# Performance work log

Measured on AMD Instinct MI355X. Metric: run time of the kernel, lower is better.

Reference implementation:

```python
import jax, jax.numpy as jnp
import numpy as np

B, D_INPUT, D_MODEL, MEM, HID, N_SYNCH, OUT_DIMS, ITERS = 128, 512, 2048, 25, 32, 256, 1000, 24
SYNC = N_SYNCH * (N_SYNCH + 1) // 2  # 32896


def setup_inputs() -> dict:
    key = jax.random.key(0)
    ks = jax.random.split(key, 12)
    inp = {
        'x': jax.random.normal(ks[0], (B, D_INPUT), jnp.float32),
        'syn_w': jax.random.normal(ks[1], (D_INPUT + D_MODEL, 2 * D_MODEL), jnp.float32) * 0.02,
        'syn_b': jnp.zeros((2 * D_MODEL,), jnp.float32),
        'ln_g': jnp.ones((D_MODEL,), jnp.float32),
        'ln_b': jnp.zeros((D_MODEL,), jnp.float32),
        'tp_w1': jax.random.normal(ks[2], (MEM, 2 * HID, D_MODEL), jnp.float32) * (1.0 / np.sqrt(MEM + 2 * HID)),
        'tp_b1': jnp.zeros((1, D_MODEL, 2 * HID), jnp.float32),
        'tp_w2': jax.random.normal(ks[3], (HID, 2, D_MODEL), jnp.float32) * (1.0 / np.sqrt(HID + 2)),
        'tp_b2': jnp.zeros((1, D_MODEL, 2), jnp.float32),
        'start_activated_state': jax.random.normal(ks[4], (D_MODEL,), jnp.float32) * (1.0 / np.sqrt(D_MODEL)),
        'start_trace': jax.random.normal(ks[5], (D_MODEL, MEM), jnp.float32) * (1.0 / np.sqrt(D_MODEL + MEM)),
        'decay_params_out': jax.random.uniform(ks[6], (SYNC,), jnp.float32),
        'out_w': jax.random.normal(ks[7], (SYNC, OUT_DIMS), jnp.float32) * 0.02,
        'out_b': jnp.zeros((OUT_DIMS,), jnp.float32),
        'idx_left': jax.random.randint(ks[8], (N_SYNCH,), 0, D_MODEL),
        'idx_right': jax.random.randint(ks[9], (N_SYNCH,), 0, D_MODEL),
        'iterations': ITERS,
    }
    return inp


def _glu(z):
    a, b = jnp.split(z, 2, axis=-1)
    return a * jax.nn.sigmoid(b)


def reference(x, syn_w, syn_b, ln_g, ln_b, tp_w1, tp_b1, tp_w2, tp_b2,
              start_activated_state, start_trace, decay_params_out, out_w, out_b,
              idx_left, idx_right, iterations):
    Bx = x.shape[0]
    D, M = start_trace.shape
    n_synch = idx_left.shape[0]
    iu, ju = np.triu_indices(n_synch)
    r = jnp.exp(-jnp.clip(decay_params_out, 0.0, 15.0))[None, :]  # (1, S)
    log_nc = np.log(out_b.shape[0]).astype(np.float32)

    def pairwise(act):  # act: (B, D) -> (B, S) upper-tri of outer product of selected neurons
        l = act[:, idx_left]
        rr = act[:, idx_right]
        outer = l[:, :, None] * rr[:, None, :]
        return outer[:, iu, ju]

    def trace_proc(trace):  # (B, D, M) -> (B, D) per-neuron MLP (NLM)
        h = _glu(jnp.einsum('BDM,MHD->BDH', trace, tp_w1) + tp_b1)
        o = _glu(jnp.einsum('BDH,HOD->BDO', h, tp_w2) + tp_b2)
        return o[..., 0]

    def layernorm(z):
        mu = jnp.mean(z, -1, keepdims=True)
        var = jnp.mean((z - mu) ** 2, -1, keepdims=True)
        return (z - mu) * jax.lax.rsqrt(var + 1e-5) * ln_g + ln_b

    act0 = jnp.broadcast_to(start_activated_state[None, :], (Bx, D))
    trace0 = jnp.broadcast_to(start_trace[None, :, :], (Bx, D, M))
    alpha0 = pairwise(act0)
    beta0 = jnp.ones_like(alpha0)

    def step(carry, _):
        trace, act, alpha, beta = carry
        pre = jnp.concatenate([x, act], axis=-1)
        state = layernorm(_glu(pre @ syn_w + syn_b))            # (B, D)
        trace = jnp.concatenate([trace[:, :, 1:], state[:, :, None]], axis=-1)
        act = trace_proc(trace)                                  # (B, D)
        pp = pairwise(act)
        alpha = r * alpha + pp
        beta = r * beta + 1.0
        sync = alpha / jnp.sqrt(beta)                            # (B, S)
        pred = sync @ out_w + out_b                              # (B, out)
        logp = jax.nn.log_softmax(pred, axis=-1)
        ne = -jnp.sum(jnp.exp(logp) * logp, axis=-1) / log_nc
        cert = jnp.stack([ne, 1.0 - ne], axis=-1)                # (B, 2)
        return (trace, act, alpha, beta), (pred, cert)

    _, (preds, certs) = jax.lax.scan(step, (trace0, act0, alpha0, beta0), None, length=iterations)
    predictions = jnp.moveaxis(preds, 0, -1)   # (B, out_dims, T)
    certainties = jnp.moveaxis(certs, 0, -1)   # (B, 2, T)
    return predictions, certainties
```

## Files before the change

### kernel.cpp

```cpp
#include <hip/hip_runtime.h>
#include <stdint.h>

#define BB      128
#define DIN     512
#define DMODEL  2048
#define MEMN    25
#define NSY     256
#define OUTD    1000
#define ITERS   24
#define SYNCN   32896
#define KPAD    33792
#define NPAD    1024
#define NSPLIT  32
#define KCH     1056
#define PREDTOT (BB*OUTD*ITERS)

typedef __attribute__((ext_vector_type(8))) short bf16x8;
typedef __attribute__((ext_vector_type(4))) float f32x4;

__device__ __forceinline__ unsigned short f2bf(float x){
    unsigned int u = __float_as_uint(x);
    u += 0x7fffu + ((u >> 16) & 1u);
    return (unsigned short)(u >> 16);
}
__device__ __forceinline__ float bf2f(unsigned short h){
    unsigned int u = ((unsigned int)h) << 16;
    return __uint_as_float(u);
}
__device__ __forceinline__ float sigm(float x){ return 1.f/(1.f + __expf(-x)); }

__device__ __forceinline__ void gload16(const unsigned short* g, unsigned short* l){
    __builtin_amdgcn_global_load_lds(
        (const __attribute__((address_space(1))) unsigned int*)(const void*)g,
        (__attribute__((address_space(3))) unsigned int*)(void*)l,
        16, 0, 0);
}

__device__ __forceinline__ void reduce_row(const float* __restrict__ part, const float* __restrict__ outb,
    float* __restrict__ dout, float* red, int b, int t, int tid){
    float v[4];
    float m = -1e30f;
#pragma unroll
    for (int q = 0; q < 4; ++q){
        int n = q*256 + tid;
        float s;
        if (n < OUTD){
            s = outb[n];
            for (int sk = 0; sk < NSPLIT; ++sk)
                s += part[(long)sk*(BB*NPAD) + (long)b*NPAD + n];
        } else s = -1e30f;
        v[q] = s;
        m = fmaxf(m, s);
    }
#pragma unroll
    for (int off = 32; off; off >>= 1) m = fmaxf(m, __shfl_down(m, off));
    int w = tid >> 6;
    if ((tid & 63) == 0) red[w] = m;
    __syncthreads();
    float M = fmaxf(fmaxf(red[0], red[1]), fmaxf(red[2], red[3]));
    __syncthreads();
    float z = 0.f, s2 = 0.f;
#pragma unroll
    for (int q = 0; q < 4; ++q){
        int n = q*256 + tid;
        if (n < OUTD){
            float e = __expf(v[q] - M);
            z += e; s2 += e*v[q];
        }
    }
#pragma unroll
    for (int off = 32; off; off >>= 1){
        z  += __shfl_down(z, off);
        s2 += __shfl_down(s2, off);
    }
    if ((tid & 63) == 0){ red[w] = z; red[4+w] = s2; }
    __syncthreads();
    if (tid == 0){
        float Z = red[0]+red[1]+red[2]+red[3];
        float S = red[4]+red[5]+red[6]+red[7];
        float logZ = M + __logf(Z);
        float ne = (logZ - S/Z) / 6.907755278982137f;
        dout[PREDTOT + b*48 + t] = ne;
        dout[PREDTOT + b*48 + 24 + t] = 1.f - ne;
    }
#pragma unroll
    for (int q = 0; q < 4; ++q){
        int n = q*256 + tid;
        if (n < OUTD) dout[(long)b*(OUTD*ITERS) + (long)n*ITERS + t] = v[q];
    }
}


__global__ __launch_bounds__(256) void init_trace_k(const float* __restrict__ st,
    unsigned short* __restrict__ trh, unsigned short* __restrict__ trl){
    const long N = (long)MEMN*DMODEL*BB;
    for (long i = (long)blockIdx.x*256 + threadIdx.x; i < N; i += (long)gridDim.x*256){
        int m = (int)(i / (DMODEL*BB));
        int rem = (int)(i % (DMODEL*BB));
        int d = rem >> 7;
        float v = st[d*MEMN + m];
        unsigned short h = f2bf(v);
        trh[i] = h;
        trl[i] = f2bf(v - bf2f(h));
    }
}

__global__ __launch_bounds__(256) void init_act_k(const float* __restrict__ sas, float* __restrict__ act){
    for (int i = blockIdx.x*256 + threadIdx.x; i < DMODEL*BB; i += gridDim.x*256)
        act[i] = sas[i >> 7];
}

__global__ __launch_bounds__(256) void init_alpha_k(const float* __restrict__ sas,
    const int* __restrict__ il, const int* __restrict__ ir, float* __restrict__ alpha){
    int i = blockIdx.x, tid = threadIdx.x;
    if (tid >= NSY - i) return;
    int j = i + tid;
    int k = i*(2*NSY - i + 1)/2 + tid;
    float a0 = sas[il[i]] * sas[ir[j]];
    for (int b = 0; b < BB; ++b) alpha[b*SYNCN + k] = a0;
}

__global__ __launch_bounds__(256) void init_rowmap_k(int* __restrict__ rowOf, int* __restrict__ rowstart){
    int i = blockIdx.x, tid = threadIdx.x;
    int start = i*(2*NSY - i + 1)/2;
    int len = NSY - i;
    if (tid == 0) rowstart[i] = start;
    for (int t = tid; t < len; t += 256) rowOf[start + t] = i;
}

__global__ __launch_bounds__(256) void transpose_f32_k(const float* __restrict__ in, float* __restrict__ out, int R, int C){
    __shared__ float S[64][65];
    int r0 = blockIdx.y*64, c0 = blockIdx.x*64;
    for (int i = threadIdx.x; i < 64*64; i += 256){
        int rr = i >> 6, cc = i & 63;
        int r = r0+rr, c = c0+cc;
        if (r < R && c < C) S[rr][cc] = in[(long)r*C + c];
    }
    __syncthreads();
    for (int i = threadIdx.x; i < 64*64; i += 256){
        int cc = i >> 6, rr = i & 63;
        int r = r0+rr, c = c0+cc;
        if (r < R && c < C) out[(long)c*R + r] = S[rr][cc];
    }
}

__global__ __launch_bounds__(256) void w1bf_prep_k(const float* __restrict__ w1t, unsigned short* __restrict__ w1bf){
    int d = blockIdx.x, tid = threadIdx.x;
    __shared__ float S[1600];
    for (int i = tid; i < 1600; i += 256) S[i] = w1t[(long)d*1600 + i];
    __syncthreads();
    for (int i = tid; i < 2048; i += 256){
        int h = i >> 5, m = i & 31;
        float v = (m < MEMN) ? S[m*64 + h] : 0.f;
        unsigned short hi = f2bf(v);
        unsigned short lo = f2bf(v - bf2f(hi));
        w1bf[(long)d*4096 + i]        = hi;
        w1bf[(long)d*4096 + 2048 + i] = lo;
    }
}

__global__ __launch_bounds__(256) void wbf_transpose_k(const float* __restrict__ w, unsigned short* __restrict__ wt){
    __shared__ float S[64][65];
    int k0 = blockIdx.x*64, n0 = blockIdx.y*64;
    int tid = threadIdx.x;
    if (k0 >= SYNCN){
        uint4 z = {0u,0u,0u,0u};
#pragma unroll
        for (int p = 0; p < 2; ++p){
            int i = tid + p*256;
            int nn = i >> 3, k8 = (i & 7)*8;
            *(uint4*)(wt + (long)(n0+nn)*KPAD + k0 + k8) = z;
        }
        return;
    }
    const long MAXI = (long)SYNCN*OUTD - 4;
#pragma unroll
    for (int p = 0; p < 4; ++p){
        int i = tid + p*256;
        int rr = i >> 4, c4 = (i & 15)*4;
        long idx = (long)(k0+rr)*OUTD + n0 + c4;
        if (idx > MAXI) idx = MAXI;
        float4 v = *(const float4*)(w + idx);
        S[rr][c4+0]=v.x; S[rr][c4+1]=v.y; S[rr][c4+2]=v.z; S[rr][c4+3]=v.w;
    }
    __syncthreads();
#pragma unroll
    for (int p = 0; p < 4; ++p){
        int i = tid + p*256;
        int nn = i >> 4, k4 = (i & 15)*4;
        ushort4 o;
        o.x = f2bf(S[k4+0][nn]); o.y = f2bf(S[k4+1][nn]);
        o.z = f2bf(S[k4+2][nn]); o.w = f2bf(S[k4+3][nn]);
        *(ushort4*)(wt + (long)(n0+nn)*KPAD + k0 + k4) = o;
    }
}

__global__ __launch_bounds__(256) void swt_convert_k(const float* __restrict__ w,
    unsigned short* __restrict__ th, unsigned short* __restrict__ tl){
    __shared__ float S[64][65];
    int k0 = blockIdx.x*64, n0 = blockIdx.y*64;
    int tid = threadIdx.x;
#pragma unroll
    for (int p = 0; p < 4; ++p){
        int i = tid + p*256;
        int rr = i >> 4, c4 = (i & 15)*4;
        float4 v = *(const float4*)(w + (long)(512 + k0 + rr)*4096 + n0 + c4);
        S[rr][c4+0]=v.x; S[rr][c4+1]=v.y; S[rr][c4+2]=v.z; S[rr][c4+3]=v.w;
    }
    __syncthreads();
#pragma unroll
    for (int p = 0; p < 4; ++p){
        int i = tid + p*256;
        int nn = i >> 4, k4 = (i & 15)*4;
        ushort4 oh, ol;
        float v0 = S[k4+0][nn], v1 = S[k4+1][nn], v2 = S[k4+2][nn], v3 = S[k4+3][nn];
        oh.x = f2bf(v0); oh.y = f2bf(v1); oh.z = f2bf(v2); oh.w = f2bf(v3);
        ol.x = f2bf(v0 - bf2f(oh.x)); ol.y = f2bf(v1 - bf2f(oh.y));
        ol.z = f2bf(v2 - bf2f(oh.z)); ol.w = f2bf(v3 - bf2f(oh.w));
        *(ushort4*)(th + (long)(n0+nn)*DMODEL + k0 + k4) = oh;
        *(ushort4*)(tl + (long)(n0+nn)*DMODEL + k0 + k4) = ol;
    }
}

__global__ __launch_bounds__(256) void act_convert_k(const float* __restrict__ act,
    unsigned short* __restrict__ th, unsigned short* __restrict__ tl){
    __shared__ float S[64][65];
    int d0 = blockIdx.x*64, b0 = blockIdx.y*64;
    int tid = threadIdx.x;
#pragma unroll
    for (int p = 0; p < 4; ++p){
        int i = tid + p*256;
        int rr = i >> 4, c4 = (i & 15)*4;
        float4 v = *(const float4*)(act + (long)(d0+rr)*BB + b0 + c4);
        S[rr][c4+0]=v.x; S[rr][c4+1]=v.y; S[rr][c4+2]=v.z; S[rr][c4+3]=v.w;
    }
    __syncthreads();
#pragma unroll
    for (int p = 0; p < 4; ++p){
        int i = tid + p*256;
        int nn = i >> 4, k4 = (i & 15)*4;
        unsigned short h[4], l[4];
#pragma unroll
        for (int q = 0; q < 4; ++q){
            float v = S[k4+q][nn];
            h[q] = f2bf(v);
            l[q] = f2bf(v - bf2f(h[q]));
        }
        *(ushort4*)(th + (long)(b0+nn)*DMODEL + d0 + k4) = ushort4{h[0],h[1],h[2],h[3]};
        *(ushort4*)(tl + (long)(b0+nn)*DMODEL + d0 + k4) = ushort4{l[0],l[1],l[2],l[3]};
    }
}

__global__ __launch_bounds__(256) void gemm_syn_k(const float* __restrict__ A, const float* __restrict__ Bw,
    const float* __restrict__ bias, float* __restrict__ out){
    int j_base = blockIdx.x*64;
    int tid = threadIdx.x;
    __shared__ float As[16][128];
    __shared__ float Bs[16][68];
    int bg = tid & 15, jg = tid >> 4;
    int b0 = bg*8, j0 = jg*4;
    float acc[8][4];
#pragma unroll
    for (int i = 0; i < 8; ++i)
#pragma unroll
        for (int q = 0; q < 4; ++q) acc[i][q] = 0.f;
    for (int kt = 0; kt < 32; ++kt){
        {
            int i0 = tid*8;
            int kk = i0 >> 7, bb = i0 & 127;
            const float4* src = (const float4*)(A + (long)(kt*16+kk)*BB + bb);
            float4 v0 = src[0], v1 = src[1];
            *(float4*)&As[kk][bb]   = v0;
            *(float4*)&As[kk][bb+4] = v1;
        }
        {
            int i0 = tid*4;
            int kk = i0 >> 6, jj = i0 & 63;
            float4 v = *(const float4*)(Bw + (long)(kt*16+kk)*4096 + j_base + jj);
            *(float4*)&Bs[kk][jj] = v;
        }
        __syncthreads();
#pragma unroll
        for (int kk = 0; kk < 16; ++kk){
            float a[8], bv[4];
            *(float4*)&a[0] = *(float4*)&As[kk][b0];
            *(float4*)&a[4] = *(float4*)&As[kk][b0+4];
            *(float4*)&bv[0] = *(float4*)&Bs[kk][j0];
#pragma unroll
            for (int i = 0; i < 8; ++i)
#pragma unroll
                for (int q = 0; q < 4; ++q) acc[i][q] += a[i]*bv[q];
        }
        __syncthreads();
    }
#pragma unroll
    for (int i = 0; i < 8; ++i){
        int bb = b0 + i;
        float4 v;
        v.x = acc[i][0]+bias[j_base+j0+0]; v.y = acc[i][1]+bias[j_base+j0+1];
        v.z = acc[i][2]+bias[j_base+j0+2]; v.w = acc[i][3]+bias[j_base+j0+3];
        *(float4*)(out + (long)bb*4096 + j_base + j0) = v;
    }
}


__global__ __launch_bounds__(256) void mfma_pair_k(
    const unsigned short* __restrict__ Ah, const unsigned short* __restrict__ Al,
    const unsigned short* __restrict__ Bh, const unsigned short* __restrict__ Bl,
    float* __restrict__ zpart,
    const unsigned short* __restrict__ Abf, const unsigned short* __restrict__ Bbf,
    float* __restrict__ part, int has_out){
    __shared__ __align__(16) unsigned short smem[12288];
    int tid = threadIdx.x;
    int bid = blockIdx.x;
    int wid = tid >> 6, lane = tid & 63;
    int wm = (wid & 1)*64, wn = (wid >> 1)*32;
    int mrow = lane & 15, kq = lane >> 4;
    int srow = tid >> 2;
    int ksg  = (tid & 3)*8;

    if (bid < 512){
        unsigned short* As_h = smem;
        unsigned short* As_l = smem + 4096;
        unsigned short* Bs_h = smem + 8192;
        unsigned short* Bs_l = smem + 10240;
        int nb = bid & 63;
        int s  = bid >> 6;

        f32x4 c[4][2];
#pragma unroll
        for (int a = 0; a < 4; ++a)
#pragma unroll
            for (int b = 0; b < 2; ++b) c[a][b] = (f32x4){0.f,0.f,0.f,0.f};

        long koff0 = (long)s*256 + ksg;
        const unsigned short* gAh1 = Ah + (long)srow*DMODEL      + koff0;
        const unsigned short* gAh2 = Ah + (long)(srow+64)*DMODEL + koff0;
        const unsigned short* gAl1 = Al + (long)srow*DMODEL      + koff0;
        const unsigned short* gAl2 = Al + (long)(srow+64)*DMODEL + koff0;
        const unsigned short* gBh  = Bh + (long)(nb*64+srow)*DMODEL + koff0;
        const unsigned short* gBl  = Bl + (long)(nb*64+srow)*DMODEL + koff0;
        unsigned short* lAh1 = As_h + wid*512;
        unsigned short* lAh2 = As_h + 2048 + wid*512;
        unsigned short* lAl1 = As_l + wid*512;
        unsigned short* lAl2 = As_l + 2048 + wid*512;
        unsigned short* lBh  = Bs_h + wid*512;
        unsigned short* lBl  = Bs_l + wid*512;

        for (int ks = 0; ks < 8; ++ks){
            int o = ks*32;
            gload16(gAh1 + o, lAh1);
            gload16(gAh2 + o, lAh2);
            gload16(gAl1 + o, lAl1);
            gload16(gAl2 + o, lAl2);
            gload16(gBh  + o, lBh);
            gload16(gBl  + o, lBl);
            __syncthreads();
            bf16x8 ah[4], al[4], bh[2], bl[2];
#pragma unroll
            for (int x = 0; x < 4; ++x){
                ah[x] = *(const bf16x8*)&As_h[(wm + x*16 + mrow)*32 + kq*8];
                al[x] = *(const bf16x8*)&As_l[(wm + x*16 + mrow)*32 + kq*8];
            }
#pragma unroll
            for (int y = 0; y < 2; ++y){
                bh[y] = *(const bf16x8*)&Bs_h[(wn + y*16 + mrow)*32 + kq*8];
                bl[y] = *(const bf16x8*)&Bs_l[(wn + y*16 + mrow)*32 + kq*8];
            }
#pragma unroll
            for (int a = 0; a < 4; ++a)
#pragma unroll
                for (int b = 0; b < 2; ++b){
                    c[a][b] = __builtin_amdgcn_mfma_f32_16x16x32_bf16(ah[a], bh[b], c[a][b], 0, 0, 0);
                    c[a][b] = __builtin_amdgcn_mfma_f32_16x16x32_bf16(al[a], bh[b], c[a][b], 0, 0, 0);
                    c[a][b] = __builtin_amdgcn_mfma_f32_16x16x32_bf16(ah[a], bl[b], c[a][b], 0, 0, 0);
                }
            __syncthreads();
        }
        float* outp = zpart + (long)s*(BB*4096);
#pragma unroll
        for (int a = 0; a < 4; ++a)
#pragma unroll
            for (int b = 0; b < 2; ++b){
                int r0 = wm + a*16 + (lane >> 4)*4;
                int col = nb*64 + wn + b*16 + (lane & 15);
#pragma unroll
                for (int reg = 0; reg < 4; ++reg)
                    outp[(long)(r0+reg)*4096 + col] = c[a][b][reg];
            }
    } else {
        if (!has_out) return;
        unsigned short* As = smem;
        unsigned short* Bs = smem + 4096;
        int idx = bid - 512;
        int sk = idx >> 4;
        int n_base = (idx & 15)*64;
        long k_base = (long)sk*KCH;

        f32x4 c[4][2];
#pragma unroll
        for (int a = 0; a < 4; ++a)
#pragma unroll
            for (int b = 0; b < 2; ++b) c[a][b] = (f32x4){0.f,0.f,0.f,0.f};

        const unsigned short* gA1 = Abf + (long)srow*KPAD      + k_base + ksg;
        const unsigned short* gA2 = Abf + (long)(srow+64)*KPAD + k_base + ksg;
        const unsigned short* gB  = Bbf + (long)(n_base+srow)*KPAD + k_base + ksg;
        unsigned short* lA1 = As + wid*512;
        unsigned short* lA2 = As + 2048 + wid*512;
        unsigned short* lB  = Bs + wid*512;

        for (int ks = 0; ks < KCH/32; ++ks){
            int o = ks*32;
            gload16(gA1 + o, lA1);
            gload16(gA2 + o, lA2);
            gload16(gB  + o, lB);
            __syncthreads();
            bf16x8 af[4], bf[2];
#pragma unroll
            for (int x = 0; x < 4; ++x)
                af[x] = *(const bf16x8*)&As[(wm + x*16 + mrow)*32 + kq*8];
#pragma unroll
            for (int y = 0; y < 2; ++y)
                bf[y] = *(const bf16x8*)&Bs[(wn + y*16 + mrow)*32 + kq*8];
#pragma unroll
            for (int a = 0; a < 4; ++a)
#pragma unroll
                for (int b = 0; b < 2; ++b)
                    c[a][b] = __builtin_amdgcn_mfma_f32_16x16x32_bf16(af[a], bf[b], c[a][b], 0, 0, 0);
            __syncthreads();
        }
        float* outp = part + (long)sk*(128*NPAD);
#pragma unroll
        for (int a = 0; a < 4; ++a)
#pragma unroll
            for (int b = 0; b < 2; ++b){
                int r0 = wm + a*16 + (lane >> 4)*4;
                int col = n_base + wn + b*16 + (lane & 15);
#pragma unroll
                for (int reg = 0; reg < 4; ++reg)
                    outp[(long)(r0+reg)*NPAD + col] = c[a][b][reg];
            }
    }
}

__global__ __launch_bounds__(1024) void glu_red_k(const float* __restrict__ C0, const float* __restrict__ zp,
    const float* __restrict__ lng, const float* __restrict__ lnb,
    unsigned short* __restrict__ trh, unsigned short* __restrict__ trl, int slot,
    const float* __restrict__ part, const float* __restrict__ outb, float* __restrict__ dout, int tprev){
    __shared__ float redA[16], redB[16];
    int tid = threadIdx.x;
    if (blockIdx.x < 128){
        int b = blockIdx.x;
        int d0 = tid*2;
        const float* base = C0 + (long)b*4096;
        float2 a = *(const float2*)(base + d0);
        float2 g = *(const float2*)(base + 2048 + d0);
#pragma unroll
        for (int s = 0; s < 8; ++s){
            const float* zb = zp + (long)s*524288 + (long)b*4096;
            float2 az = *(const float2*)(zb + d0);
            float2 gz = *(const float2*)(zb + 2048 + d0);
            a.x += az.x; a.y += az.y; g.x += gz.x; g.y += gz.y;
        }
        float v0 = a.x*sigm(g.x), v1 = a.y*sigm(g.y);
        float s1 = v0+v1, s2 = v0*v0+v1*v1;
#pragma unroll
        for (int off = 32; off; off >>= 1){
            s1 += __shfl_down(s1, off);
            s2 += __shfl_down(s2, off);
        }
        if ((tid & 63) == 0){ redA[tid>>6] = s1; redB[tid>>6] = s2; }
        __syncthreads();
        if (tid == 0){
            float sa = 0.f, sb = 0.f;
            for (int i = 0; i < 16; ++i){ sa += redA[i]; sb += redB[i]; }
            float mu = sa*(1.f/2048.f);
            float var = sb*(1.f/2048.f) - mu*mu;
            redA[0] = mu;
            redB[0] = rsqrtf(var + 1e-5f);
        }
        __syncthreads();
        float mu = redA[0], inv = redB[0];
        float st0 = (v0-mu)*inv*lng[d0]   + lnb[d0];
        float st1 = (v1-mu)*inv*lng[d0+1] + lnb[d0+1];
        unsigned short h0 = f2bf(st0), h1 = f2bf(st1);
        long o0 = ((long)slot*DMODEL + d0)*BB + b;
        trh[o0]      = h0;  trl[o0]      = f2bf(st0 - bf2f(h0));
        trh[o0 + BB] = h1;  trl[o0 + BB] = f2bf(st1 - bf2f(h1));
    } else {
        if (tprev < 0) return;
        int b = blockIdx.x - 128;
        float v = -1e30f;
        if (tid < OUTD){
            float s = outb[tid];
            for (int sk = 0; sk < NSPLIT; ++sk)
                s += part[(long)sk*(BB*NPAD) + (long)b*NPAD + tid];
            v = s;
        }
        float m = v;
#pragma unroll
        for (int off = 32; off; off >>= 1) m = fmaxf(m, __shfl_down(m, off));
        if ((tid & 63) == 0) redA[tid>>6] = m;
        __syncthreads();
        if (tid == 0){
            float r = redA[0];
            for (int i = 1; i < 16; ++i) r = fmaxf(r, redA[i]);
            redA[0] = r;
        }
        __syncthreads();
        float M = redA[0];
        __syncthreads();
        float e  = (tid < OUTD) ? __expf(v - M) : 0.f;
        float ev = e * ((tid < OUTD) ? v : 0.f);
        float z = e, s2 = ev;
#pragma unroll
        for (int off = 32; off; off >>= 1){
            z  += __shfl_down(z, off);
            s2 += __shfl_down(s2, off);
        }
        if ((tid & 63) == 0){ redA[tid>>6] = z; redB[tid>>6] = s2; }
        __syncthreads();
        if (tid == 0){
            float Z = 0.f, S = 0.f;
            for (int i = 0; i < 16; ++i){ Z += redA[i]; S += redB[i]; }
            float logZ = M + __logf(Z);
            float ne = (logZ - S/Z) / 6.907755278982137f;
            dout[PREDTOT + b*48 + tprev] = ne;
            dout[PREDTOT + b*48 + 24 + tprev] = 1.f - ne;
        }
        if (tid < OUTD) dout[(long)b*(OUTD*ITERS) + (long)tid*ITERS + tprev] = v;
    }
}

__global__ __launch_bounds__(256) void trace_proc_k(
    const unsigned short* __restrict__ trh, const unsigned short* __restrict__ trl,
    const unsigned short* __restrict__ w1bf,
    const float* __restrict__ b1, const float* __restrict__ w2t, const float* __restrict__ b2,
    float* __restrict__ act, unsigned short* __restrict__ aTh, unsigned short* __restrict__ aTl, int t){
    int d = blockIdx.x, tid = threadIdx.x;
    __shared__ __align__(16) unsigned short Ah[128*40];
    __shared__ __align__(16) unsigned short Al[128*40];
    __shared__ __align__(16) unsigned short Bbuf[4096];
    __shared__ float hh[128*33];
    __shared__ float w2s[64];

    for (int i = tid; i < MEMN*64; i += 256){
        int m = i >> 6, bp = i & 63;
        int phys = t + 1 + m; if (phys >= MEMN) phys -= MEMN; if (phys >= MEMN) phys -= MEMN;
        long gaddr = ((long)phys*DMODEL + d)*BB + bp*2;
        ushort2 vh = *(const ushort2*)(trh + gaddr);
        ushort2 vl = *(const ushort2*)(trl + gaddr);
        Ah[(bp*2+0)*40 + m] = vh.x; Ah[(bp*2+1)*40 + m] = vh.y;
        Al[(bp*2+0)*40 + m] = vl.x; Al[(bp*2+1)*40 + m] = vl.y;
    }
    for (int i = tid; i < 7*128; i += 256){
        int m = MEMN + (i >> 7), b = i & 127;
        Ah[b*40 + m] = 0; Al[b*40 + m] = 0;
    }
    {
        const uint4* src = (const uint4*)(w1bf + (long)d*4096);
        uint4* dst = (uint4*)Bbuf;
        for (int i = tid; i < 512; i += 256) dst[i] = src[i];
    }
    if (tid < 64) w2s[tid] = w2t[(long)d*64 + tid];
    __syncthreads();

    int wid = tid >> 6, lane = tid & 63;
    int mrow = lane & 15, kq = lane >> 4;
    bf16x8 ahf[2], alf[2], bhf[4], blf[4];
#pragma unroll
    for (int bt = 0; bt < 2; ++bt){
        int r = (wid*2 + bt)*16 + mrow;
        ahf[bt] = *(const bf16x8*)&Ah[r*40 + kq*8];
        alf[bt] = *(const bf16x8*)&Al[r*40 + kq*8];
    }
#pragma unroll
    for (int ht = 0; ht < 4; ++ht){
        int r = ht*16 + mrow;
        bhf[ht] = *(const bf16x8*)&Bbuf[r*32 + kq*8];
        blf[ht] = *(const bf16x8*)&Bbuf[2048 + r*32 + kq*8];
    }
    f32x4 c[2][4];
#pragma unroll
    for (int bt = 0; bt < 2; ++bt)
#pragma unroll
        for (int ht = 0; ht < 4; ++ht){
            c[bt][ht] = (f32x4){0.f,0.f,0.f,0.f};
            c[bt][ht] = __builtin_amdgcn_mfma_f32_16x16x32_bf16(ahf[bt], bhf[ht], c[bt][ht], 0, 0, 0);
            c[bt][ht] = __builtin_amdgcn_mfma_f32_16x16x32_bf16(alf[bt], bhf[ht], c[bt][ht], 0, 0, 0);
            c[bt][ht] = __builtin_amdgcn_mfma_f32_16x16x32_bf16(ahf[bt], blf[ht], c[bt][ht], 0, 0, 0);
        }
    int quad = lane >> 4;
#pragma unroll
    for (int bt = 0; bt < 2; ++bt){
        int bb0 = (wid*2 + bt)*16 + quad*4;
#pragma unroll
        for (int ht = 0; ht < 2; ++ht){
            int h = ht*16 + (lane & 15);
            float ba = b1[(long)d*64 + h];
            float bg = b1[(long)d*64 + 32 + h];
#pragma unroll
            for (int reg = 0; reg < 4; ++reg){
                float a = c[bt][ht][reg] + ba;
                float g = c[bt][ht+2][reg] + bg;
                hh[(bb0+reg)*33 + h] = a * sigm(g);
            }
        }
    }
    __syncthreads();
    if (tid < 128){
        int bb = tid;
        float o0 = b2[(long)d*2+0], o1 = b2[(long)d*2+1];
#pragma unroll
        for (int h = 0; h < 32; ++h){
            float hv = hh[bb*33 + h];
            o0 += hv * w2s[h*2+0];
            o1 += hv * w2s[h*2+1];
        }
        float a = o0 * sigm(o1);
        act[(long)d*BB + bb] = a;
        unsigned short h16 = f2bf(a);
        aTh[(long)bb*DMODEL + d] = h16;
        aTl[(long)bb*DMODEL + d] = f2bf(a - bf2f(h16));
    }
}

__global__ __launch_bounds__(256) void pairwise_sync_k(const float* __restrict__ act, const float* __restrict__ decay,
    const int* __restrict__ il, const int* __restrict__ ir,
    const int* __restrict__ rowOf, const int* __restrict__ rowstart,
    float* __restrict__ alpha, unsigned short* __restrict__ syncb, int t){
    int k = blockIdx.x*256 + threadIdx.x;
    int bg = blockIdx.y;
    int blo = bg*32, bhi = blo + 32;
    if (k >= SYNCN){
        if (k < KPAD)
            for (int b = blo; b < bhi; ++b) syncb[(long)b*KPAD + k] = 0;
        return;
    }
    int i = rowOf[k];
    int j = i + (k - rowstart[i]);
    float cc = fminf(fmaxf(decay[k], 0.f), 15.f);
    float r = __expf(-cc);
    float bet;
    if (cc < 1e-30f) bet = (float)(t + 2);
    else {
        float e1 = expm1f(-cc);
        float et = expm1f(-cc*(float)(t+1));
        bet = 1.f + et + et/e1;
    }
    float rs = rsqrtf(bet);
    const float* aL = act + (long)il[i]*BB;
    const float* aR = act + (long)ir[j]*BB;
    for (int b = blo; b < bhi; ++b){
        float pp = aL[b]*aR[b];
        float al = r*alpha[(long)b*SYNCN + k] + pp;
        alpha[(long)b*SYNCN + k] = al;
        syncb[(long)b*KPAD + k] = f2bf(al*rs);
    }
}

__global__ __launch_bounds__(256) void out_gemm_k(const unsigned short* __restrict__ Abf,
    const unsigned short* __restrict__ Bbf, float* __restrict__ part){
    int n_base = blockIdx.x*64;
    int sk = blockIdx.y;
    int tid = threadIdx.x;
    int wid = tid >> 6, lane = tid & 63;
    int wm = (wid & 1)*64, wn = (wid >> 1)*32;
    long k_base = (long)sk*KCH;
    __shared__ __align__(16) unsigned short As[128*32];
    __shared__ __align__(16) unsigned short Bs[64*32];
    f32x4 c[4][2];
#pragma unroll
    for (int a = 0; a < 4; ++a)
#pragma unroll
        for (int b = 0; b < 2; ++b) c[a][b] = (f32x4){0.f,0.f,0.f,0.f};

    int mrow = lane & 15, kq = lane >> 4;
    int srow = tid >> 2;
    int ksg  = (tid & 3)*8;
    const unsigned short* gA1 = Abf + (long)srow*KPAD      + k_base + ksg;
    const unsigned short* gA2 = Abf + (long)(srow+64)*KPAD + k_base + ksg;
    const unsigned short* gB  = Bbf + (long)(n_base+srow)*KPAD + k_base + ksg;
    unsigned short* lA1 = As + wid*512;
    unsigned short* lA2 = As + 2048 + wid*512;
    unsigned short* lB  = Bs + wid*512;

    for (int ks = 0; ks < KCH/32; ++ks){
        int o = ks*32;
        gload16(gA1 + o, lA1);
        gload16(gA2 + o, lA2);
        gload16(gB  + o, lB);
        __syncthreads();
        bf16x8 af[4], bf[2];
#pragma unroll
        for (int x = 0; x < 4; ++x)
            af[x] = *(const bf16x8*)&As[(wm + x*16 + mrow)*32 + kq*8];
#pragma unroll
        for (int y = 0; y < 2; ++y)
            bf[y] = *(const bf16x8*)&Bs[(wn + y*16 + mrow)*32 + kq*8];
#pragma unroll
        for (int a = 0; a < 4; ++a)
#pragma unroll
            for (int b = 0; b < 2; ++b)
                c[a][b] = __builtin_amdgcn_mfma_f32_16x16x32_bf16(af[a], bf[b], c[a][b], 0, 0, 0);
        __syncthreads();
    }
    float* outp = part + (long)sk*(128*NPAD);
#pragma unroll
    for (int a = 0; a < 4; ++a)
#pragma unroll
        for (int b = 0; b < 2; ++b){
            int r0 = wm + a*16 + (lane >> 4)*4;
            int col = n_base + wn + b*16 + (lane & 15);
#pragma unroll
            for (int reg = 0; reg < 4; ++reg)
                outp[(long)(r0+reg)*NPAD + col] = c[a][b][reg];
        }
}

__global__ __launch_bounds__(256) void reduce_final_k(const float* __restrict__ part,
    const float* __restrict__ outb, float* __restrict__ dout){
    __shared__ float red[8];
    reduce_row(part, outb, dout, red, blockIdx.x, ITERS-1, threadIdx.x);
}


extern "C" void kernel_launch(void* const* d_in, const int* in_sizes, int n_in,
                              void* d_out, int out_size, void* d_ws, size_t ws_size,
                              hipStream_t stream){
    const float* x      = (const float*)d_in[0];
    const float* syn_w  = (const float*)d_in[1];
    const float* syn_b  = (const float*)d_in[2];
    const float* ln_g   = (const float*)d_in[3];
    const float* ln_b   = (const float*)d_in[4];
    const float* tp_w1  = (const float*)d_in[5];
    const float* tp_b1  = (const float*)d_in[6];
    const float* tp_w2  = (const float*)d_in[7];
    const float* tp_b2  = (const float*)d_in[8];
    const float* sas    = (const float*)d_in[9];
    const float* strc   = (const float*)d_in[10];
    const float* decay  = (const float*)d_in[11];
    const float* out_w  = (const float*)d_in[12];
    const float* out_b  = (const float*)d_in[13];
    const int*   il     = (const int*)d_in[14];
    const int*   ir     = (const int*)d_in[15];
    float* dout = (float*)d_out;

    char* ws = (char*)d_ws;
    size_t off = 0;
    auto alloc = [&](size_t bytes)->void*{
        void* p = ws + off;
        off += (bytes + 255) & ~(size_t)255;
        return p;
    };
    unsigned short* trh = (unsigned short*)alloc((size_t)MEMN*DMODEL*BB*2);
    unsigned short* trl = (unsigned short*)alloc((size_t)MEMN*DMODEL*BB*2);
    float* act     = (float*)alloc((size_t)DMODEL*BB*4);
    float* C0      = (float*)alloc((size_t)BB*4096*4);
    float* xt      = (float*)alloc((size_t)DIN*BB*4);
    float* w2t     = (float*)alloc((size_t)DMODEL*64*4);
    unsigned short* w1bf = (unsigned short*)alloc((size_t)DMODEL*4096*2);
    float* alpha   = (float*)alloc((size_t)BB*SYNCN*4);
    unsigned short* syncb = (unsigned short*)alloc((size_t)BB*KPAD*2);
    unsigned short* wbt   = (unsigned short*)alloc((size_t)NPAD*KPAD*2);
    float* part    = (float*)alloc((size_t)NSPLIT*BB*NPAD*4);
    float* w1t     = part;
    float* zpart   = (float*)alloc((size_t)8*BB*4096*4);
    unsigned short* swT_h = (unsigned short*)alloc((size_t)4096*DMODEL*2);
    unsigned short* swT_l = (unsigned short*)alloc((size_t)4096*DMODEL*2);
    unsigned short* aT_h  = (unsigned short*)alloc((size_t)BB*DMODEL*2);
    unsigned short* aT_l  = (unsigned short*)alloc((size_t)BB*DMODEL*2);
    int* rowOf    = (int*)alloc((size_t)SYNCN*4);
    int* rowstart = (int*)alloc((size_t)NSY*4);
    (void)ws_size; (void)in_sizes; (void)n_in; (void)out_size;

    init_trace_k<<<8192, 256, 0, stream>>>(strc, trh, trl);
    init_act_k<<<1024, 256, 0, stream>>>(sas, act);
    init_alpha_k<<<256, 256, 0, stream>>>(sas, il, ir, alpha);
    init_rowmap_k<<<256, 256, 0, stream>>>(rowOf, rowstart);
    transpose_f32_k<<<dim3(32, 25), 256, 0, stream>>>(tp_w1, w1t, 1600, 2048);
    w1bf_prep_k<<<2048, 256, 0, stream>>>(w1t, w1bf);
    transpose_f32_k<<<dim3(32, 1),  256, 0, stream>>>(tp_w2, w2t, 64, 2048);
    transpose_f32_k<<<dim3(8, 2),   256, 0, stream>>>(x, xt, 128, 512);
    wbf_transpose_k<<<dim3(KPAD/64, 16), 256, 0, stream>>>(out_w, wbt);
    swt_convert_k<<<dim3(32, 64), 256, 0, stream>>>(syn_w, swT_h, swT_l);
    gemm_syn_k<<<64, 256, 0, stream>>>(xt, syn_w, syn_b, C0);
    act_convert_k<<<dim3(32, 2), 256, 0, stream>>>(act, aT_h, aT_l);

    for (int t = 0; t < ITERS; ++t){
        mfma_pair_k<<<1024, 256, 0, stream>>>(aT_h, aT_l, swT_h, swT_l, zpart,
                                              syncb, wbt, part, t > 0);
        glu_red_k<<<256, 1024, 0, stream>>>(C0, zpart, ln_g, ln_b, trh, trl, t % MEMN,
                                            part, out_b, dout, t - 1);
        trace_proc_k<<<2048, 256, 0, stream>>>(trh, trl, w1bf, tp_b1, w2t, tp_b2, act, aT_h, aT_l, t);
        pairwise_sync_k<<<dim3(KPAD/256, 4), 256, 0, stream>>>(act, decay, il, ir, rowOf, rowstart, alpha, syncb, t);
    }
    out_gemm_k<<<dim3(16, NSPLIT), 256, 0, stream>>>(syncb, wbt, part);
    reduce_final_k<<<128, 256, 0, stream>>>(part, out_b, dout);
}
```

Before: 2.582 ms.

## Regroup per-iteration kernels into three fused launches pairing independent stages

Each iteration now runs three launches instead of four. The first pairs the output GEMM for the previous step with the GLU+layernorm stage. The second pairs the previous step's softmax reduction with trace processing. The third pairs the next step's synapse GEMM with the pairwise sync update. This needs a prologue launch that computes the synapse GEMM for the first step and skips the GEMM on the last step. The aim is to cut launch count and let independent work share the GPU, at the cost of mixed block types per launch and more complex step indexing.

```diff
diff --git a/kernel.cpp b/kernel.cpp
--- a/kernel.cpp
+++ b/kernel.cpp
@@ -303,27 +303,261 @@
     }
 }
 
-
-__global__ __launch_bounds__(256) void mfma_pair_k(
+__global__ __launch_bounds__(256) void d1_out_glu_k(
+    const unsigned short* __restrict__ Abf, const unsigned short* __restrict__ Bbf,
+    float* __restrict__ part,
+    const float* __restrict__ C0, const float* __restrict__ zp,
+    const float* __restrict__ lng, const float* __restrict__ lnb,
+    unsigned short* __restrict__ trh, unsigned short* __restrict__ trl,
+    int slot, int do_out){
+    __shared__ __align__(16) char U[24576];
+    int tid = threadIdx.x;
+    int bid = blockIdx.x;
+    if (bid < 512){
+        if (!do_out) return;
+        unsigned short* As = (unsigned short*)U;
+        unsigned short* Bs = (unsigned short*)(U + 8192);
+        int wid = tid >> 6, lane = tid & 63;
+        int wm = (wid & 1)*64, wn = (wid >> 1)*32;
+        int mrow = lane & 15, kq = lane >> 4;
+        int srow = tid >> 2;
+        int ksg  = (tid & 3)*8;
+        int sk = bid >> 4;
+        int n_base = (bid & 15)*64;
+        long k_base = (long)sk*KCH;
+
+        f32x4 c[4][2];
+#pragma unroll
+        for (int a = 0; a < 4; ++a)
+#pragma unroll
+            for (int b = 0; b < 2; ++b) c[a][b] = (f32x4){0.f,0.f,0.f,0.f};
+
+        const unsigned short* gA1 = Abf + (long)srow*KPAD      + k_base + ksg;
+        const unsigned short* gA2 = Abf + (long)(srow+64)*KPAD + k_base + ksg;
+        const unsigned short* gB  = Bbf + (long)(n_base+srow)*KPAD + k_base + ksg;
+        unsigned short* lA1 = As + wid*512;
+        unsigned short* lA2 = As + 2048 + wid*512;
+        unsigned short* lB  = Bs + wid*512;
+
+        for (int ks = 0; ks < KCH/32; ++ks){
+            int o = ks*32;
+            gload16(gA1 + o, lA1);
+            gload16(gA2 + o, lA2);
+            gload16(gB  + o, lB);
+            __syncthreads();
+            bf16x8 af[4], bf[2];
+#pragma unroll
+            for (int x = 0; x < 4; ++x)
+                af[x] = *(const bf16x8*)&As[(wm + x*16 + mrow)*32 + kq*8];
+#pragma unroll
+            for (int y = 0; y < 2; ++y)
+                bf[y] = *(const bf16x8*)&Bs[(wn + y*16 + mrow)*32 + kq*8];
+#pragma unroll
+            for (int a = 0; a < 4; ++a)
+#pragma unroll
+                for (int b = 0; b < 2; ++b)
+                    c[a][b] = __builtin_amdgcn_mfma_f32_16x16x32_bf16(af[a], bf[b], c[a][b], 0, 0, 0);
+            __syncthreads();
+        }
+        float* outp = part + (long)sk*(128*NPAD);
+#pragma unroll
+        for (int a = 0; a < 4; ++a)
+#pragma unroll
+            for (int b = 0; b < 2; ++b){
+                int r0 = wm + a*16 + (lane >> 4)*4;
+                int col = n_base + wn + b*16 + (lane & 15);
+#pragma unroll
+                for (int reg = 0; reg < 4; ++reg)
+                    outp[(long)(r0+reg)*NPAD + col] = c[a][b][reg];
+            }
+    } else {
+        float* redA = (float*)U;
+        float* redB = (float*)(U + 16);
+        int b = bid - 512;
+        int d0 = tid*8;
+        const float* base = C0 + (long)b*4096;
+        float4 a0 = *(const float4*)(base + d0);
+        float4 a1 = *(const float4*)(base + d0 + 4);
+        float4 g0 = *(const float4*)(base + 2048 + d0);
+        float4 g1 = *(const float4*)(base + 2048 + d0 + 4);
+#pragma unroll
+        for (int s = 0; s < 8; ++s){
+            const float* zb = zp + (long)s*524288 + (long)b*4096;
+            float4 z0 = *(const float4*)(zb + d0);
+            float4 z1 = *(const float4*)(zb + d0 + 4);
+            float4 y0 = *(const float4*)(zb + 2048 + d0);
+            float4 y1 = *(const float4*)(zb + 2048 + d0 + 4);
+            a0.x+=z0.x; a0.y+=z0.y; a0.z+=z0.z; a0.w+=z0.w;
+            a1.x+=z1.x; a1.y+=z1.y; a1.z+=z1.z; a1.w+=z1.w;
+            g0.x+=y0.x; g0.y+=y0.y; g0.z+=y0.z; g0.w+=y0.w;
+            g1.x+=y1.x; g1.y+=y1.y; g1.z+=y1.z; g1.w+=y1.w;
+        }
+        float v[8];
+        v[0]=a0.x*sigm(g0.x); v[1]=a0.y*sigm(g0.y); v[2]=a0.z*sigm(g0.z); v[3]=a0.w*sigm(g0.w);
+        v[4]=a1.x*sigm(g1.x); v[5]=a1.y*sigm(g1.y); v[6]=a1.z*sigm(g1.z); v[7]=a1.w*sigm(g1.w);
+        float s1 = 0.f, s2 = 0.f;
+#pragma unroll
+        for (int i = 0; i < 8; ++i){ s1 += v[i]; s2 += v[i]*v[i]; }
+#pragma unroll
+        for (int off = 32; off; off >>= 1){
+            s1 += __shfl_down(s1, off);
+            s2 += __shfl_down(s2, off);
+        }
+        int w = tid >> 6;
+        if ((tid & 63) == 0){ redA[w] = s1; redB[w] = s2; }
+        __syncthreads();
+        if (tid == 0){
+            float sa = redA[0]+redA[1]+redA[2]+redA[3];
+            float sb = redB[0]+redB[1]+redB[2]+redB[3];
+            float mu = sa*(1.f/2048.f);
+            float var = sb*(1.f/2048.f) - mu*mu;
+            redA[0] = mu;
+            redB[0] = rsqrtf(var + 1e-5f);
+        }
+        __syncthreads();
+        float mu = redA[0], inv = redB[0];
+        float4 lg0 = *(const float4*)(lng + d0);
+        float4 lg1 = *(const float4*)(lng + d0 + 4);
+        float4 lb0 = *(const float4*)(lnb + d0);
+        float4 lb1 = *(const float4*)(lnb + d0 + 4);
+        float gg[8] = {lg0.x,lg0.y,lg0.z,lg0.w,lg1.x,lg1.y,lg1.z,lg1.w};
+        float bb[8] = {lb0.x,lb0.y,lb0.z,lb0.w,lb1.x,lb1.y,lb1.z,lb1.w};
+        long obase = ((long)slot*DMODEL + d0)*BB + b;
+#pragma unroll
+        for (int i = 0; i < 8; ++i){
+            float st = (v[i]-mu)*inv*gg[i] + bb[i];
+            unsigned short h = f2bf(st);
+            trh[obase + (long)i*BB] = h;
+            trl[obase + (long)i*BB] = f2bf(st - bf2f(h));
+        }
+    }
+}
+
+__global__ __launch_bounds__(256) void d2_red_trace_k(
+    const float* __restrict__ part, const float* __restrict__ outb, float* __restrict__ dout,
+    const unsigned short* __restrict__ trh, const unsigned short* __restrict__ trl,
+    const unsigned short* __restrict__ w1bf,
+    const float* __restrict__ b1, const float* __restrict__ w2t, const float* __restrict__ b2,
+    float* __restrict__ act, unsigned short* __restrict__ aTh, unsigned short* __restrict__ aTl,
+    int t){
+    __shared__ __align__(16) char U[45824];
+    int tid = threadIdx.x;
+    int bid = blockIdx.x;
+    if (bid < 128){
+        if (t <= 0) return;
+        reduce_row(part, outb, dout, (float*)U, bid, t - 1, tid);
+    } else {
+        int d = bid - 128;
+        unsigned short* Ah   = (unsigned short*)U;
+        unsigned short* Al   = (unsigned short*)(U + 10240);
+        unsigned short* Bbuf = (unsigned short*)(U + 20480);
+        float* hh  = (float*)(U + 28672);
+        float* w2s = (float*)(U + 45568);
+
+        for (int i = tid; i < MEMN*64; i += 256){
+            int m = i >> 6, bp = i & 63;
+            int phys = t + 1 + m; if (phys >= MEMN) phys -= MEMN; if (phys >= MEMN) phys -= MEMN;
+            long gaddr = ((long)phys*DMODEL + d)*BB + bp*2;
+            ushort2 vh = *(const ushort2*)(trh + gaddr);
+            ushort2 vl = *(const ushort2*)(trl + gaddr);
+            Ah[(bp*2+0)*40 + m] = vh.x; Ah[(bp*2+1)*40 + m] = vh.y;
+            Al[(bp*2+0)*40 + m] = vl.x; Al[(bp*2+1)*40 + m] = vl.y;
+        }
+        for (int i = tid; i < 7*128; i += 256){
+            int m = MEMN + (i >> 7), b = i & 127;
+            Ah[b*40 + m] = 0; Al[b*40 + m] = 0;
+        }
+        {
+            const uint4* src = (const uint4*)(w1bf + (long)d*4096);
+            uint4* dst = (uint4*)Bbuf;
+            for (int i = tid; i < 512; i += 256) dst[i] = src[i];
+        }
+        if (tid < 64) w2s[tid] = w2t[(long)d*64 + tid];
+        __syncthreads();
+
+        int wid = tid >> 6, lane = tid & 63;
+        int mrow = lane & 15, kq = lane >> 4;
+        bf16x8 ahf[2], alf[2], bhf[4], blf[4];
+#pragma unroll
+        for (int bt = 0; bt < 2; ++bt){
+            int r = (wid*2 + bt)*16 + mrow;
+            ahf[bt] = *(const bf16x8*)&Ah[r*40 + kq*8];
+            alf[bt] = *(const bf16x8*)&Al[r*40 + kq*8];
+        }
+#pragma unroll
+        for (int ht = 0; ht < 4; ++ht){
+            int r = ht*16 + mrow;
+            bhf[ht] = *(const bf16x8*)&Bbuf[r*32 + kq*8];
+            blf[ht] = *(const bf16x8*)&Bbuf[2048 + r*32 + kq*8];
+        }
+        f32x4 c[2][4];
+#pragma unroll
+        for (int bt = 0; bt < 2; ++bt)
+#pragma unroll
+            for (int ht = 0; ht < 4; ++ht){
+                c[bt][ht] = (f32x4){0.f,0.f,0.f,0.f};
+                c[bt][ht] = __builtin_amdgcn_mfma_f32_16x16x32_bf16(ahf[bt], bhf[ht], c[bt][ht], 0, 0, 0);
+                c[bt][ht] = __builtin_amdgcn_mfma_f32_16x16x32_bf16(alf[bt], bhf[ht], c[bt][ht], 0, 0, 0);
+                c[bt][ht] = __builtin_amdgcn_mfma_f32_16x16x32_bf16(ahf[bt], blf[ht], c[bt][ht], 0, 0, 0);
+            }
+        int quad = lane >> 4;
+#pragma unroll
+        for (int bt = 0; bt < 2; ++bt){
+            int bb0 = (wid*2 + bt)*16 + quad*4;
+#pragma unroll
+            for (int ht = 0; ht < 2; ++ht){
+                int h = ht*16 + (lane & 15);
+                float ba = b1[(long)d*64 + h];
+                float bg = b1[(long)d*64 + 32 + h];
+#pragma unroll
+                for (int reg = 0; reg < 4; ++reg){
+                    float a = c[bt][ht][reg] + ba;
+                    float g = c[bt][ht+2][reg] + bg;
+                    hh[(bb0+reg)*33 + h] = a * sigm(g);
+                }
+            }
+        }
+        __syncthreads();
+        if (tid < 128){
+            int bb = tid;
+            float o0 = b2[(long)d*2+0], o1 = b2[(long)d*2+1];
+#pragma unroll
+            for (int h = 0; h < 32; ++h){
+                float hv = hh[bb*33 + h];
+                o0 += hv * w2s[h*2+0];
+                o1 += hv * w2s[h*2+1];
+            }
+            float a = o0 * sigm(o1);
+            act[(long)d*BB + bb] = a;
+            unsigned short h16 = f2bf(a);
+            aTh[(long)bb*DMODEL + d] = h16;
+            aTl[(long)bb*DMODEL + d] = f2bf(a - bf2f(h16));
+        }
+    }
+}
+
+__global__ __launch_bounds__(256) void d3_syn_pair_k(
     const unsigned short* __restrict__ Ah, const unsigned short* __restrict__ Al,
     const unsigned short* __restrict__ Bh, const unsigned short* __restrict__ Bl,
     float* __restrict__ zpart,
-    const unsigned short* __restrict__ Abf, const unsigned short* __restrict__ Bbf,
-    float* __restrict__ part, int has_out){
-    __shared__ __align__(16) unsigned short smem[12288];
+    const float* __restrict__ act, const float* __restrict__ decay,
+    const int* __restrict__ il, const int* __restrict__ ir,
+    const int* __restrict__ rowOf, const int* __restrict__ rowstart,
+    float* __restrict__ alpha, unsigned short* __restrict__ syncb, int t){
+    __shared__ __align__(16) char U[24576];
     int tid = threadIdx.x;
     int bid = blockIdx.x;
-    int wid = tid >> 6, lane = tid & 63;
-    int wm = (wid & 1)*64, wn = (wid >> 1)*32;
-    int mrow = lane & 15, kq = lane >> 4;
-    int srow = tid >> 2;
-    int ksg  = (tid & 3)*8;
-
     if (bid < 512){
-        unsigned short* As_h = smem;
-        unsigned short* As_l = smem + 4096;
-        unsigned short* Bs_h = smem + 8192;
-        unsigned short* Bs_l = smem + 10240;
+        if (t >= ITERS-1) return;
+        unsigned short* As_h = (unsigned short*)U;
+        unsigned short* As_l = (unsigned short*)(U + 8192);
+        unsigned short* Bs_h = (unsigned short*)(U + 16384);
+        unsigned short* Bs_l = (unsigned short*)(U + 20480);
+        int wid = tid >> 6, lane = tid & 63;
+        int wm = (wid & 1)*64, wn = (wid >> 1)*32;
+        int mrow = lane & 15, kq = lane >> 4;
+        int srow = tid >> 2;
+        int ksg  = (tid & 3)*8;
         int nb = bid & 63;
         int s  = bid >> 6;
 
@@ -389,274 +623,37 @@
                     outp[(long)(r0+reg)*4096 + col] = c[a][b][reg];
             }
     } else {
-        if (!has_out) return;
-        unsigned short* As = smem;
-        unsigned short* Bs = smem + 4096;
+        if (t < 0) return;
         int idx = bid - 512;
-        int sk = idx >> 4;
-        int n_base = (idx & 15)*64;
-        long k_base = (long)sk*KCH;
-
-        f32x4 c[4][2];
-#pragma unroll
-        for (int a = 0; a < 4; ++a)
-#pragma unroll
-            for (int b = 0; b < 2; ++b) c[a][b] = (f32x4){0.f,0.f,0.f,0.f};
-
-        const unsigned short* gA1 = Abf + (long)srow*KPAD      + k_base + ksg;
-        const unsigned short* gA2 = Abf + (long)(srow+64)*KPAD + k_base + ksg;
-        const unsigned short* gB  = Bbf + (long)(n_base+srow)*KPAD + k_base + ksg;
-        unsigned short* lA1 = As + wid*512;
-        unsigned short* lA2 = As + 2048 + wid*512;
-        unsigned short* lB  = Bs + wid*512;
-
-        for (int ks = 0; ks < KCH/32; ++ks){
-            int o = ks*32;
-            gload16(gA1 + o, lA1);
-            gload16(gA2 + o, lA2);
-            gload16(gB  + o, lB);
-            __syncthreads();
-            bf16x8 af[4], bf[2];
-#pragma unroll
-            for (int x = 0; x < 4; ++x)
-                af[x] = *(const bf16x8*)&As[(wm + x*16 + mrow)*32 + kq*8];
-#pragma unroll
-            for (int y = 0; y < 2; ++y)
-                bf[y] = *(const bf16x8*)&Bs[(wn + y*16 + mrow)*32 + kq*8];
-#pragma unroll
-            for (int a = 0; a < 4; ++a)
-#pragma unroll
-                for (int b = 0; b < 2; ++b)
-                    c[a][b] = __builtin_amdgcn_mfma_f32_16x16x32_bf16(af[a], bf[b], c[a][b], 0, 0, 0);
-            __syncthreads();
-        }
-        float* outp = part + (long)sk*(128*NPAD);
-#pragma unroll
-        for (int a = 0; a < 4; ++a)
-#pragma unroll
-            for (int b = 0; b < 2; ++b){
-                int r0 = wm + a*16 + (lane >> 4)*4;
-                int col = n_base + wn + b*16 + (lane & 15);
-#pragma unroll
-                for (int reg = 0; reg < 4; ++reg)
-                    outp[(long)(r0+reg)*NPAD + col] = c[a][b][reg];
-            }
-    }
-}
-
-__global__ __launch_bounds__(1024) void glu_red_k(const float* __restrict__ C0, const float* __restrict__ zp,
-    const float* __restrict__ lng, const float* __restrict__ lnb,
-    unsigned short* __restrict__ trh, unsigned short* __restrict__ trl, int slot,
-    const float* __restrict__ part, const float* __restrict__ outb, float* __restrict__ dout, int tprev){
-    __shared__ float redA[16], redB[16];
-    int tid = threadIdx.x;
-    if (blockIdx.x < 128){
-        int b = blockIdx.x;
-        int d0 = tid*2;
-        const float* base = C0 + (long)b*4096;
-        float2 a = *(const float2*)(base + d0);
-        float2 g = *(const float2*)(base + 2048 + d0);
-#pragma unroll
-        for (int s = 0; s < 8; ++s){
-            const float* zb = zp + (long)s*524288 + (long)b*4096;
-            float2 az = *(const float2*)(zb + d0);
-            float2 gz = *(const float2*)(zb + 2048 + d0);
-            a.x += az.x; a.y += az.y; g.x += gz.x; g.y += gz.y;
-        }
-        float v0 = a.x*sigm(g.x), v1 = a.y*sigm(g.y);
-        float s1 = v0+v1, s2 = v0*v0+v1*v1;
-#pragma unroll
-        for (int off = 32; off; off >>= 1){
-            s1 += __shfl_down(s1, off);
-            s2 += __shfl_down(s2, off);
-        }
-        if ((tid & 63) == 0){ redA[tid>>6] = s1; redB[tid>>6] = s2; }
-        __syncthreads();
-        if (tid == 0){
-            float sa = 0.f, sb = 0.f;
-            for (int i = 0; i < 16; ++i){ sa += redA[i]; sb += redB[i]; }
-            float mu = sa*(1.f/2048.f);
-            float var = sb*(1.f/2048.f) - mu*mu;
-            redA[0] = mu;
-            redB[0] = rsqrtf(var + 1e-5f);
-        }
-        __syncthreads();
-        float mu = redA[0], inv = redB[0];
-        float st0 = (v0-mu)*inv*lng[d0]   + lnb[d0];
-        float st1 = (v1-mu)*inv*lng[d0+1] + lnb[d0+1];
-        unsigned short h0 = f2bf(st0), h1 = f2bf(st1);
-        long o0 = ((long)slot*DMODEL + d0)*BB + b;
-        trh[o0]      = h0;  trl[o0]      = f2bf(st0 - bf2f(h0));
-        trh[o0 + BB] = h1;  trl[o0 + BB] = f2bf(st1 - bf2f(h1));
-    } else {
-        if (tprev < 0) return;
-        int b = blockIdx.x - 128;
-        float v = -1e30f;
-        if (tid < OUTD){
-            float s = outb[tid];
-            for (int sk = 0; sk < NSPLIT; ++sk)
-                s += part[(long)sk*(BB*NPAD) + (long)b*NPAD + tid];
-            v = s;
-        }
-        float m = v;
-#pragma unroll
-        for (int off = 32; off; off >>= 1) m = fmaxf(m, __shfl_down(m, off));
-        if ((tid & 63) == 0) redA[tid>>6] = m;
-        __syncthreads();
-        if (tid == 0){
-            float r = redA[0];
-            for (int i = 1; i < 16; ++i) r = fmaxf(r, redA[i]);
-            redA[0] = r;
-        }
-        __syncthreads();
-        float M = redA[0];
-        __syncthreads();
-        float e  = (tid < OUTD) ? __expf(v - M) : 0.f;
-        float ev = e * ((tid < OUTD) ? v : 0.f);
-        float z = e, s2 = ev;
-#pragma unroll
-        for (int off = 32; off; off >>= 1){
-            z  += __shfl_down(z, off);
-            s2 += __shfl_down(s2, off);
-        }
-        if ((tid & 63) == 0){ redA[tid>>6] = z; redB[tid>>6] = s2; }
-        __syncthreads();
-        if (tid == 0){
-            float Z = 0.f, S = 0.f;
-            for (int i = 0; i < 16; ++i){ Z += redA[i]; S += redB[i]; }
-            float logZ = M + __logf(Z);
-            float ne = (logZ - S/Z) / 6.907755278982137f;
-            dout[PREDTOT + b*48 + tprev] = ne;
-            dout[PREDTOT + b*48 + 24 + tprev] = 1.f - ne;
-        }
-        if (tid < OUTD) dout[(long)b*(OUTD*ITERS) + (long)tid*ITERS + tprev] = v;
-    }
-}
-
-__global__ __launch_bounds__(256) void trace_proc_k(
-    const unsigned short* __restrict__ trh, const unsigned short* __restrict__ trl,
-    const unsigned short* __restrict__ w1bf,
-    const float* __restrict__ b1, const float* __restrict__ w2t, const float* __restrict__ b2,
-    float* __restrict__ act, unsigned short* __restrict__ aTh, unsigned short* __restrict__ aTl, int t){
-    int d = blockIdx.x, tid = threadIdx.x;
-    __shared__ __align__(16) unsigned short Ah[128*40];
-    __shared__ __align__(16) unsigned short Al[128*40];
-    __shared__ __align__(16) unsigned short Bbuf[4096];
-    __shared__ float hh[128*33];
-    __shared__ float w2s[64];
-
-    for (int i = tid; i < MEMN*64; i += 256){
-        int m = i >> 6, bp = i & 63;
-        int phys = t + 1 + m; if (phys >= MEMN) phys -= MEMN; if (phys >= MEMN) phys -= MEMN;
-        long gaddr = ((long)phys*DMODEL + d)*BB + bp*2;
-        ushort2 vh = *(const ushort2*)(trh + gaddr);
-        ushort2 vl = *(const ushort2*)(trl + gaddr);
-        Ah[(bp*2+0)*40 + m] = vh.x; Ah[(bp*2+1)*40 + m] = vh.y;
-        Al[(bp*2+0)*40 + m] = vl.x; Al[(bp*2+1)*40 + m] = vl.y;
-    }
-    for (int i = tid; i < 7*128; i += 256){
-        int m = MEMN + (i >> 7), b = i & 127;
-        Ah[b*40 + m] = 0; Al[b*40 + m] = 0;
-    }
-    {
-        const uint4* src = (const uint4*)(w1bf + (long)d*4096);
-        uint4* dst = (uint4*)Bbuf;
-        for (int i = tid; i < 512; i += 256) dst[i] = src[i];
-    }
-    if (tid < 64) w2s[tid] = w2t[(long)d*64 + tid];
-    __syncthreads();
-
-    int wid = tid >> 6, lane = tid & 63;
-    int mrow = lane & 15, kq = lane >> 4;
-    bf16x8 ahf[2], alf[2], bhf[4], blf[4];
-#pragma unroll
-    for (int bt = 0; bt < 2; ++bt){
-        int r = (wid*2 + bt)*16 + mrow;
-        ahf[bt] = *(const bf16x8*)&Ah[r*40 + kq*8];
-        alf[bt] = *(const bf16x8*)&Al[r*40 + kq*8];
-    }
-#pragma unroll
-    for (int ht = 0; ht < 4; ++ht){
-        int r = ht*16 + mrow;
-        bhf[ht] = *(const bf16x8*)&Bbuf[r*32 + kq*8];
-        blf[ht] = *(const bf16x8*)&Bbuf[2048 + r*32 + kq*8];
-    }
-    f32x4 c[2][4];
-#pragma unroll
-    for (int bt = 0; bt < 2; ++bt)
-#pragma unroll
-        for (int ht = 0; ht < 4; ++ht){
-            c[bt][ht] = (f32x4){0.f,0.f,0.f,0.f};
-            c[bt][ht] = __builtin_amdgcn_mfma_f32_16x16x32_bf16(ahf[bt], bhf[ht], c[bt][ht], 0, 0, 0);
-            c[bt][ht] = __builtin_amdgcn_mfma_f32_16x16x32_bf16(alf[bt], bhf[ht], c[bt][ht], 0, 0, 0);
-            c[bt][ht] = __builtin_amdgcn_mfma_f32_16x16x32_bf16(ahf[bt], blf[ht], c[bt][ht], 0, 0, 0);
-        }
-    int quad = lane >> 4;
-#pragma unroll
-    for (int bt = 0; bt < 2; ++bt){
-        int bb0 = (wid*2 + bt)*16 + quad*4;
-#pragma unroll
-        for (int ht = 0; ht < 2; ++ht){
-            int h = ht*16 + (lane & 15);
-            float ba = b1[(long)d*64 + h];
-            float bg = b1[(long)d*64 + 32 + h];
-#pragma unroll
-            for (int reg = 0; reg < 4; ++reg){
-                float a = c[bt][ht][reg] + ba;
-                float g = c[bt][ht+2][reg] + bg;
-                hh[(bb0+reg)*33 + h] = a * sigm(g);
-            }
-        }
-    }
-    __syncthreads();
-    if (tid < 128){
-        int bb = tid;
-        float o0 = b2[(long)d*2+0], o1 = b2[(long)d*2+1];
-#pragma unroll
-        for (int h = 0; h < 32; ++h){
-            float hv = hh[bb*33 + h];
-            o0 += hv * w2s[h*2+0];
-            o1 += hv * w2s[h*2+1];
-        }
-        float a = o0 * sigm(o1);
-        act[(long)d*BB + bb] = a;
-        unsigned short h16 = f2bf(a);
-        aTh[(long)bb*DMODEL + d] = h16;
-        aTl[(long)bb*DMODEL + d] = f2bf(a - bf2f(h16));
-    }
-}
-
-__global__ __launch_bounds__(256) void pairwise_sync_k(const float* __restrict__ act, const float* __restrict__ decay,
-    const int* __restrict__ il, const int* __restrict__ ir,
-    const int* __restrict__ rowOf, const int* __restrict__ rowstart,
-    float* __restrict__ alpha, unsigned short* __restrict__ syncb, int t){
-    int k = blockIdx.x*256 + threadIdx.x;
-    int bg = blockIdx.y;
-    int blo = bg*32, bhi = blo + 32;
-    if (k >= SYNCN){
-        if (k < KPAD)
-            for (int b = blo; b < bhi; ++b) syncb[(long)b*KPAD + k] = 0;
-        return;
-    }
-    int i = rowOf[k];
-    int j = i + (k - rowstart[i]);
-    float cc = fminf(fmaxf(decay[k], 0.f), 15.f);
-    float r = __expf(-cc);
-    float bet;
-    if (cc < 1e-30f) bet = (float)(t + 2);
-    else {
-        float e1 = expm1f(-cc);
-        float et = expm1f(-cc*(float)(t+1));
-        bet = 1.f + et + et/e1;
-    }
-    float rs = rsqrtf(bet);
-    const float* aL = act + (long)il[i]*BB;
-    const float* aR = act + (long)ir[j]*BB;
-    for (int b = blo; b < bhi; ++b){
-        float pp = aL[b]*aR[b];
-        float al = r*alpha[(long)b*SYNCN + k] + pp;
-        alpha[(long)b*SYNCN + k] = al;
-        syncb[(long)b*KPAD + k] = f2bf(al*rs);
+        int xx = idx % 132;
+        int bg = idx / 132;
+        int k = xx*256 + tid;
+        int blo = bg*32, bhi = blo + 32;
+        if (k >= SYNCN){
+            if (k < KPAD)
+                for (int b = blo; b < bhi; ++b) syncb[(long)b*KPAD + k] = 0;
+            return;
+        }
+        int i = rowOf[k];
+        int j = i + (k - rowstart[i]);
+        float cc = fminf(fmaxf(decay[k], 0.f), 15.f);
+        float r = __expf(-cc);
+        float bet;
+        if (cc < 1e-30f) bet = (float)(t + 2);
+        else {
+            float e1 = expm1f(-cc);
+            float et = expm1f(-cc*(float)(t+1));
+            bet = 1.f + et + et/e1;
+        }
+        float rs = rsqrtf(bet);
+        const float* aL = act + (long)il[i]*BB;
+        const float* aR = act + (long)ir[j]*BB;
+        for (int b = blo; b < bhi; ++b){
+            float pp = aL[b]*aR[b];
+            float al = r*alpha[(long)b*SYNCN + k] + pp;
+            alpha[(long)b*SYNCN + k] = al;
+            syncb[(long)b*KPAD + k] = f2bf(al*rs);
+        }
     }
 }
 
@@ -788,13 +785,20 @@
     gemm_syn_k<<<64, 256, 0, stream>>>(xt, syn_w, syn_b, C0);
     act_convert_k<<<dim3(32, 2), 256, 0, stream>>>(act, aT_h, aT_l);
 
+    d3_syn_pair_k<<<1040, 256, 0, stream>>>(aT_h, aT_l, swT_h, swT_l, zpart,
+                                            act, decay, il, ir, rowOf, rowstart,
+                                            alpha, syncb, -1);
+
     for (int t = 0; t < ITERS; ++t){
-        mfma_pair_k<<<1024, 256, 0, stream>>>(aT_h, aT_l, swT_h, swT_l, zpart,
-                                              syncb, wbt, part, t > 0);
-        glu_red_k<<<256, 1024, 0, stream>>>(C0, zpart, ln_g, ln_b, trh, trl, t % MEMN,
-                                            part, out_b, dout, t - 1);
-        trace_proc_k<<<2048, 256, 0, stream>>>(trh, trl, w1bf, tp_b1, w2t, tp_b2, act, aT_h, aT_l, t);
-        pairwise_sync_k<<<dim3(KPAD/256, 4), 256, 0, stream>>>(act, decay, il, ir, rowOf, rowstart, alpha, syncb, t);
+        d1_out_glu_k<<<640, 256, 0, stream>>>(syncb, wbt, part,
+                                              C0, zpart, ln_g, ln_b, trh, trl,
+                                              t % MEMN, t > 0);
+        d2_red_trace_k<<<2176, 256, 0, stream>>>(part, out_b, dout,
+                                                 trh, trl, w1bf, tp_b1, w2t, tp_b2,
+                                                 act, aT_h, aT_l, t);
+        d3_syn_pair_k<<<1040, 256, 0, stream>>>(aT_h, aT_l, swT_h, swT_l, zpart,
+                                                act, decay, il, ir, rowOf, rowstart,
+                                                alpha, syncb, t);
     }
     out_gemm_k<<<dim3(16, NSPLIT), 256, 0, stream>>>(syncb, wbt, part);
     reduce_final_k<<<128, 256, 0, stream>>>(part, out_b, dout);
```

Result: faster. 2.423 ms (median of 2 runs) (-6.2%).
